# Optimization experiments

Measured on AMD Instinct MI355X. Metric: run time of the kernel, lower is better.

## Reference

```python
import jax, jax.numpy as jnp
import numpy as np

B, P, V, L = 256, 512, 8, 16
N = B * P            # 131072 nodes
C = V * L            # 128 in_channels (== out_channels, forced by the .view in forward)
H = 4                # heads
DOUT = 128           # out_channels per head
E = N * 5            # k=5 neighbors per node
NEG_SLOPE = 0.2


def setup_inputs() -> dict:
    key = jax.random.key(0)
    ks = jax.random.split(key, 8)
    patches = jax.random.normal(ks[0], (B, P, V, L), dtype=jnp.float32)
    edge_index = jax.random.randint(ks[1], (2, E), 0, N, dtype=jnp.int64)
    s = 1.0 / np.sqrt(C)
    W_gat = jax.random.uniform(ks[2], (C, H * DOUT), dtype=jnp.float32, minval=-s, maxval=s)
    att_src = jax.random.uniform(ks[3], (H, DOUT), dtype=jnp.float32, minval=-s, maxval=s)
    att_dst = jax.random.uniform(ks[4], (H, DOUT), dtype=jnp.float32, minval=-s, maxval=s)
    bias_gat = jnp.zeros((H * DOUT,), dtype=jnp.float32)
    s2 = 1.0 / np.sqrt(H * DOUT)
    W_lin = jax.random.uniform(ks[5], (H * DOUT, DOUT), dtype=jnp.float32, minval=-s2, maxval=s2)
    b_lin = jax.random.uniform(ks[6], (DOUT,), dtype=jnp.float32, minval=-s2, maxval=s2)
    return {"patches": patches, "edge_index": edge_index, "W_gat": W_gat,
            "att_src": att_src, "att_dst": att_dst, "bias_gat": bias_gat,
            "W_lin": W_lin, "b_lin": b_lin}


def reference(patches, edge_index, W_gat, att_src, att_dst, bias_gat, W_lin, b_lin):
    b, p, v, l = patches.shape
    n = b * p
    x = patches.reshape(n, v * l)                      # [N, C]
    xw = (x @ W_gat).reshape(n, H, DOUT)               # [N, H, D]
    # PyG GATConv default add_self_loops=True
    loops = jnp.arange(n, dtype=edge_index.dtype)
    src = jnp.concatenate([edge_index[0], loops])      # message source j
    dst = jnp.concatenate([edge_index[1], loops])      # message target i
    a_src = jnp.einsum('nhd,hd->nh', xw, att_src)      # [N, H]
    a_dst = jnp.einsum('nhd,hd->nh', xw, att_dst)
    e = jax.nn.leaky_relu(a_src[src] + a_dst[dst], NEG_SLOPE)   # [Etot, H]
    m = jax.ops.segment_max(e, dst, num_segments=n)
    ex = jnp.exp(e - m[dst])
    denom = jax.ops.segment_sum(ex, dst, num_segments=n)
    alpha = ex / (denom[dst] + 1e-16)                  # segment softmax over in-edges
    out = jax.ops.segment_sum(alpha[:, :, None] * xw[src], dst, num_segments=n)  # [N, H, D]
    out = out.reshape(n, H * DOUT) + bias_gat
    out = jax.nn.elu(out)
    out = out @ W_lin + b_lin                          # [N, DOUT]
    return out.reshape(b, p, v, l)
```

## Files before the change

### kernel.cpp

```cpp
#include <hip/hip_runtime.h>
#include <hip/hip_bf16.h>
#include <stdint.h>

#define N_NODES 131072
#define C_IN    128
#define HEADS   4
#define DHEAD   128
#define HD      512
#define E_EDGES 655360
#define NEG_SLOPE 0.2f
#define NCHUNK  4
#define CHUNK_N (N_NODES / NCHUNK)
#define SCAN_B  (N_NODES / 256)

typedef short bf16x8 __attribute__((ext_vector_type(8)));
typedef float f32x4  __attribute__((ext_vector_type(4)));

__device__ __forceinline__ float bf2f(unsigned short u) {
    unsigned int x = ((unsigned int)u) << 16;
    return __builtin_bit_cast(float, x);
}
__device__ __forceinline__ unsigned short f2bf(float f) {
    unsigned int u = __builtin_bit_cast(unsigned int, f);
    unsigned int r = u + 0x7FFFu + ((u >> 16) & 1u);
    return (unsigned short)(r >> 16);
}
__device__ __forceinline__ float lrelu(float v) {
    return v > 0.0f ? v : NEG_SLOPE * v;
}

__device__ __forceinline__ int perm512(int s) {
    int w = s >> 7, r = s & 127;
    int P = r >> 5, half = (r >> 3) & 3, b = (r >> 2) & 1, e = r & 3;
    return w * 128 + (2 * P + b) * 16 + half * 4 + e;
}

__global__ void detect_kernel(const unsigned int* p_f, const unsigned int* p_i, int* flags) {
    int lane = threadIdx.x;
    int cnt = 0;
#pragma unroll
    for (int r = 0; r < 4; r++) {
        unsigned int e = (p_f[lane + 64 * r] >> 7) & 0xFFu;
        cnt += (e >= 110u && e <= 137u) ? 1 : 0;
    }
    int z = 0;
#pragma unroll
    for (int r = 0; r < 2; r++) {
        z += (p_i[2 * (lane + 64 * r) + 1] == 0u) ? 1 : 0;
    }
#pragma unroll
    for (int o = 1; o < 64; o <<= 1) {
        cnt += __shfl_xor(cnt, o, 64);
        z   += __shfl_xor(z, o, 64);
    }
    if (lane == 0) {
        flags[0] = (cnt >= 128) ? 1 : 0;
        flags[1] = (z == 128) ? 1 : 0;
    }
}

__global__ void conv_w1(const void* in, unsigned short* out, const int* flags) {
    int idx = blockIdx.x * blockDim.x + threadIdx.x;
    int e = idx & 7;
    int l = (idx >> 3) & 63;
    int t = idx >> 9;
    int kk = t & 3, g = t >> 2;
    int col = g * 16 + (l & 15);
    int k = kk * 32 + (l >> 4) * 8 + e;
    float v = flags[0] ? bf2f(((const unsigned short*)in)[k * HD + col])
                       : ((const float*)in)[k * HD + col];
    out[idx] = f2bf(v);
}

__global__ void conv_w2(const void* in, unsigned short* out, const int* flags) {
    int idx = blockIdx.x * blockDim.x + threadIdx.x;
    int n = idx >> 9, s = idx & 511;
    int k = perm512(s);
    float v = flags[0] ? bf2f(((const unsigned short*)in)[k * DHEAD + n])
                       : ((const float*)in)[k * DHEAD + n];
    out[idx] = f2bf(v);
}

__global__ void conv_small(const void* as, const void* ad, const void* bg, const void* bl,
                           float* att_s, float* att_d, float* bias_g, float* b_lin,
                           const int* flags) {
    int i = blockIdx.x * blockDim.x + threadIdx.x;
    bool bf = flags[0] != 0;
    if (i < 512) {
        att_s[i] = bf ? bf2f(((const unsigned short*)as)[i]) : ((const float*)as)[i];
    } else if (i < 1024) {
        int j = i - 512;
        att_d[j] = bf ? bf2f(((const unsigned short*)ad)[j]) : ((const float*)ad)[j];
    } else if (i < 1536) {
        int j = perm512(i - 1024);
        bias_g[i - 1024] = bf ? bf2f(((const unsigned short*)bg)[j]) : ((const float*)bg)[j];
    } else if (i < 1664) {
        int j = i - 1536;
        b_lin[j] = bf ? bf2f(((const unsigned short*)bl)[j]) : ((const float*)bl)[j];
    }
}

__global__ void conv_edges_hist(const void* in, int* src32, int* dst32, int* deg,
                                const int* flags) {
    int i = blockIdx.x * blockDim.x + threadIdx.x;
    if (i >= 2 * E_EDGES) return;
    int v = flags[1] ? (int)((const long long*)in)[i] : ((const int*)in)[i];
    if (i < E_EDGES) {
        src32[i] = v;
    } else {
        dst32[i - E_EDGES] = v;
        atomicAdd(&deg[v], 1);
    }
}

__global__ void zero_deg(int* deg) {
    int i = blockIdx.x * blockDim.x + threadIdx.x;
    deg[i] = 0;
}

__global__ void scan_local(const int* __restrict__ deg, int* __restrict__ offv,
                           int* __restrict__ bsums) {
    __shared__ int tmp[256];
    int t = threadIdx.x;
    int g = blockIdx.x * 256 + t;
    int v = deg[g];
    tmp[t] = v;
    __syncthreads();
#pragma unroll
    for (int d = 1; d < 256; d <<= 1) {
        int x = (t >= d) ? tmp[t - d] : 0;
        __syncthreads();
        tmp[t] += x;
        __syncthreads();
    }
    offv[g] = tmp[t] - v;
    if (t == 255) bsums[blockIdx.x] = tmp[t];
}

__global__ void scan_bsums(int* bsums) {
    __shared__ int tmp[SCAN_B];
    int t = threadIdx.x;
    int v = bsums[t];
    tmp[t] = v;
    __syncthreads();
#pragma unroll
    for (int d = 1; d < SCAN_B; d <<= 1) {
        int x = (t >= d) ? tmp[t - d] : 0;
        __syncthreads();
        tmp[t] += x;
        __syncthreads();
    }
    bsums[t] = tmp[t] - v;
}

__global__ void scan_apply(int* __restrict__ offv, const int* __restrict__ bsums,
                           int* __restrict__ cursor) {
    int g = blockIdx.x * 256 + threadIdx.x;
    int v = offv[g] + bsums[blockIdx.x];
    offv[g] = v;
    cursor[g] = v;
}

__global__ void scatter_kernel(const int* src32, const int* dst32, int* cursor, int* csr) {
    int i = blockIdx.x * blockDim.x + threadIdx.x;
    int d = dst32[i];
    int pos = atomicAdd(&cursor[d], 1);
    csr[pos] = src32[i];
}

__launch_bounds__(256)
__global__ void gemm1_fused(const void* __restrict__ Ain,
                            const unsigned short* __restrict__ BT2,
                            const float* __restrict__ attS, const float* __restrict__ attD,
                            unsigned short* __restrict__ xw,
                            float* __restrict__ aSrc, float* __restrict__ aDst,
                            const int* __restrict__ flags) {
    __shared__ unsigned short lA[64 * 136];
    int tid = threadIdx.x;
    int m0 = blockIdx.x * 64;

    if (flags[0] == 0) {
        const float* Af = (const float*)Ain;
#pragma unroll
        for (int p = 0; p < 8; p++) {
            int l = p * 256 + tid;
            int r = l >> 5, c = (l & 31) * 4;
            float4 f = *(const float4*)&Af[(size_t)(m0 + r) * C_IN + c];
            unsigned short t4[4] = {f2bf(f.x), f2bf(f.y), f2bf(f.z), f2bf(f.w)};
            *(uint2*)&lA[r * 136 + c] = *(const uint2*)t4;
        }
    } else {
        const unsigned short* Ab = (const unsigned short*)Ain;
#pragma unroll
        for (int p = 0; p < 4; p++) {
            int l = p * 256 + tid;
            int r = l >> 4, c = (l & 15) * 8;
            *(uint4*)&lA[r * 136 + c] = *(const uint4*)&Ab[(size_t)(m0 + r) * C_IN + c];
        }
    }
    __syncthreads();

    int w = tid >> 6, lane = tid & 63;
    int lr = lane & 15, half = lane >> 4;

    bf16x8 afr[4][4];
#pragma unroll
    for (int i = 0; i < 4; i++)
#pragma unroll
        for (int kk = 0; kk < 4; kk++)
            afr[i][kk] = *(const bf16x8*)&lA[(i * 16 + lr) * 136 + kk * 32 + half * 8];

    const float4* attS4 = (const float4*)attS;
    const float4* attD4 = (const float4*)attD;

    float dS[4], dD[4];
#pragma unroll
    for (int i = 0; i < 4; i++) { dS[i] = 0.f; dD[i] = 0.f; }

    bf16x8 bbuf[2][4];
#pragma unroll
    for (int kk = 0; kk < 4; kk++)
        bbuf[0][kk] = *(const bf16x8*)&BT2[(((w * 8 + 0) * 4 + kk) << 9) + (lane << 3)];

    uint2 pk_lo[4];

#pragma unroll
    for (int p = 0; p < 8; p++) {
        int cur = p & 1;
        if (p < 7) {
#pragma unroll
            for (int kk = 0; kk < 4; kk++)
                bbuf[cur ^ 1][kk] =
                    *(const bf16x8*)&BT2[(((w * 8 + p + 1) * 4 + kk) << 9) + (lane << 3)];
        }

        f32x4 acc[4];
#pragma unroll
        for (int i = 0; i < 4; i++) acc[i] = (f32x4){0.f, 0.f, 0.f, 0.f};

#pragma unroll
        for (int kk = 0; kk < 4; kk++)
#pragma unroll
            for (int i = 0; i < 4; i++)
                acc[i] = __builtin_amdgcn_mfma_f32_16x16x32_bf16(bbuf[cur][kk], afr[i][kk], acc[i], 0, 0, 0);

        float4 s4 = attS4[w * 32 + p * 4 + half];
        float4 d4 = attD4[w * 32 + p * 4 + half];
#pragma unroll
        for (int i = 0; i < 4; i++) {
            dS[i] += acc[i][0] * s4.x + acc[i][1] * s4.y + acc[i][2] * s4.z + acc[i][3] * s4.w;
            dD[i] += acc[i][0] * d4.x + acc[i][1] * d4.y + acc[i][2] * d4.z + acc[i][3] * d4.w;
        }

        if ((p & 1) == 0) {
#pragma unroll
            for (int i = 0; i < 4; i++) {
                pk_lo[i].x = (unsigned int)f2bf(acc[i][0]) | ((unsigned int)f2bf(acc[i][1]) << 16);
                pk_lo[i].y = (unsigned int)f2bf(acc[i][2]) | ((unsigned int)f2bf(acc[i][3]) << 16);
            }
        } else {
            int P = p >> 1;
#pragma unroll
            for (int i = 0; i < 4; i++) {
                uint4 q;
                q.x = pk_lo[i].x;
                q.y = pk_lo[i].y;
                q.z = (unsigned int)f2bf(acc[i][0]) | ((unsigned int)f2bf(acc[i][1]) << 16);
                q.w = (unsigned int)f2bf(acc[i][2]) | ((unsigned int)f2bf(acc[i][3]) << 16);
                *(uint4*)&xw[(size_t)(m0 + i * 16 + lr) * HD + w * 128 + P * 32 + half * 8] = q;
            }
        }
    }

#pragma unroll
    for (int i = 0; i < 4; i++) {
        float ps = dS[i], pd = dD[i];
        ps += __shfl_xor(ps, 16, 64);
        ps += __shfl_xor(ps, 32, 64);
        pd += __shfl_xor(pd, 16, 64);
        pd += __shfl_xor(pd, 32, 64);
        if (half == 0) {
            aSrc[(size_t)(m0 + i * 16 + lr) * HEADS + w] = ps;
            aDst[(size_t)(m0 + i * 16 + lr) * HEADS + w] = pd;
        }
    }
}

__launch_bounds__(256)
__global__ void gemm2(const unsigned short* __restrict__ A,
                      const unsigned short* __restrict__ BT,
                      const float* __restrict__ bias,
                      unsigned short* Cbf, float* Cf,
                      const int* __restrict__ flags, long long rowOff) {
    __shared__ unsigned short smem[64 * 136];
    unsigned short* lA = smem;
    unsigned short* lB = smem + 64 * 40;
    int tid = threadIdx.x;
    int m0 = blockIdx.x * 64;
    int wid = tid >> 6, lane = tid & 63;
    int wr = (wid >> 1) * 32, wc = (wid & 1) * 64;
    int lr = lane & 15, half = lane >> 4;

    f32x4 acc[2][4];
#pragma unroll
    for (int i = 0; i < 2; i++)
#pragma unroll
        for (int j = 0; j < 4; j++) acc[i][j] = (f32x4){0.f, 0.f, 0.f, 0.f};

    for (int k0 = 0; k0 < HD; k0 += 32) {
        {
            int r = tid >> 2, c = (tid & 3) * 8;
            *(uint4*)&lA[r * 40 + c] = *(const uint4*)&A[(size_t)(m0 + r) * HD + k0 + c];
        }
#pragma unroll
        for (int p = 0; p < 2; p++) {
            int l = p * 256 + tid;
            int r = l >> 2, c = (l & 3) * 8;
            *(uint4*)&lB[r * 40 + c] = *(const uint4*)&BT[(size_t)r * HD + k0 + c];
        }
        __syncthreads();
        bf16x8 af[2], bfr[4];
#pragma unroll
        for (int i = 0; i < 2; i++)
            af[i] = *(const bf16x8*)&lA[(wr + i * 16 + lr) * 40 + half * 8];
#pragma unroll
        for (int j = 0; j < 4; j++)
            bfr[j] = *(const bf16x8*)&lB[(wc + j * 16 + lr) * 40 + half * 8];
#pragma unroll
        for (int i = 0; i < 2; i++)
#pragma unroll
            for (int j = 0; j < 4; j++)
                acc[i][j] = __builtin_amdgcn_mfma_f32_16x16x32_bf16(af[i], bfr[j], acc[i][j], 0, 0, 0);
        __syncthreads();
    }

    if (flags[0] != 0) {
#pragma unroll
        for (int i = 0; i < 2; i++)
#pragma unroll
            for (int j = 0; j < 4; j++) {
                int gcol = wc + j * 16 + lr;
                float b = bias[gcol];
#pragma unroll
                for (int r = 0; r < 4; r++)
                    smem[(wr + i * 16 + half * 4 + r) * 136 + gcol] = f2bf(acc[i][j][r] + b);
            }
        __syncthreads();
#pragma unroll
        for (int p = 0; p < 2; p++) {
            int l = p * 256 + tid;
            int r = l >> 4, c = (l & 15) * 8;
            *(uint4*)&Cbf[(size_t)(rowOff + m0 + r) * DHEAD + c] = *(const uint4*)&smem[r * 136 + c];
        }
    } else {
#pragma unroll
        for (int i = 0; i < 2; i++)
#pragma unroll
            for (int j = 0; j < 4; j++) {
                int gcol = wc + j * 16 + lr;
                float b = bias[gcol];
#pragma unroll
                for (int r = 0; r < 4; r++) {
                    int grow = m0 + wr + i * 16 + half * 4 + r;
                    Cf[(size_t)(rowOff + grow) * DHEAD + gcol] = acc[i][j][r] + b;
                }
            }
    }
}

__launch_bounds__(256)
__global__ void aggregate(const unsigned short* __restrict__ xw,
                          const float* __restrict__ a_src, const float* __restrict__ a_dst,
                          const int* __restrict__ off, const int* __restrict__ deg,
                          const int* __restrict__ csr, const float* __restrict__ bias_g,
                          unsigned short* __restrict__ y, int nodeBase) {
    int local = blockIdx.x * 4 + (threadIdx.x >> 6);
    int node = nodeBase + local;
    int l = threadIdx.x & 63;
    int h = l >> 4;
    int ebase = l * 8;
    int o = off[node], dn = deg[node];
    float ad = a_dst[node * HEADS + h];

    float acc[8];
    float denom;
    {
        float w = __expf(lrelu(a_src[node * HEADS + h] + ad));
        uint4 q = *(const uint4*)&xw[(size_t)node * HD + ebase];
        const unsigned short* u = (const unsigned short*)&q;
        denom = w;
#pragma unroll
        for (int k = 0; k < 8; k++) acc[k] = w * bf2f(u[k]);
    }

    for (int e0 = 0; e0 < dn; e0 += 8) {
        int   idx[8];
        float as[8];
        uint4 px[8];
#pragma unroll
        for (int b = 0; b < 8; b++)
            idx[b] = (e0 + b < dn) ? csr[o + e0 + b] : node;
#pragma unroll
        for (int b = 0; b < 8; b++)
            as[b] = a_src[idx[b] * HEADS + h];
#pragma unroll
        for (int b = 0; b < 8; b++)
            px[b] = *(const uint4*)&xw[(size_t)idx[b] * HD + ebase];
#pragma unroll
        for (int b = 0; b < 8; b++) {
            float w = (e0 + b < dn) ? __expf(lrelu(as[b] + ad)) : 0.0f;
            denom += w;
            const unsigned short* u = (const unsigned short*)&px[b];
#pragma unroll
            for (int k = 0; k < 8; k++) acc[k] += w * bf2f(u[k]);
        }
    }

    float inv = 1.0f / (denom + 1e-16f);
    unsigned short outp[8];
#pragma unroll
    for (int k = 0; k < 8; k++) {
        float v = acc[k] * inv + bias_g[ebase + k];
        v = v > 0.f ? v : (__expf(v) - 1.0f);
        outp[k] = f2bf(v);
    }
    *(uint4*)&y[(size_t)local * HD + ebase] = *(const uint4*)outp;
}

extern "C" void kernel_launch(void* const* d_in, const int* in_sizes, int n_in,
                              void* d_out, int out_size, void* d_ws, size_t ws_size,
                              hipStream_t stream) {
    char* ws = (char*)d_ws;
    size_t wsoff = 0;
    auto alloc = [&](size_t bytes) -> char* {
        char* p = ws + wsoff;
        wsoff += (bytes + 255) & ~(size_t)255;
        return p;
    };

    int*            flags  = (int*)           alloc(256);
    unsigned short* WT1    = (unsigned short*)alloc((size_t)HD * C_IN * 2);
    unsigned short* WT2    = (unsigned short*)alloc((size_t)DHEAD * HD * 2);
    float*          attS   = (float*)         alloc(HD * 4);
    float*          attD   = (float*)         alloc(HD * 4);
    float*          biasG  = (float*)         alloc(HD * 4);
    float*          bLin   = (float*)         alloc(DHEAD * 4);
    int*            src32  = (int*)           alloc((size_t)E_EDGES * 4);
    int*            dst32  = (int*)           alloc((size_t)E_EDGES * 4);
    int*            deg    = (int*)           alloc((size_t)N_NODES * 4);
    int*            offv   = (int*)           alloc((size_t)(N_NODES + 1) * 4);
    int*            cursor = (int*)           alloc((size_t)N_NODES * 4);
    int*            csr    = (int*)           alloc((size_t)E_EDGES * 4);
    int*            bsums  = (int*)           alloc((size_t)SCAN_B * 4);
    float*          aSrc   = (float*)         alloc((size_t)N_NODES * HEADS * 4);
    float*          aDst   = (float*)         alloc((size_t)N_NODES * HEADS * 4);
    unsigned short* xw     = (unsigned short*)alloc((size_t)N_NODES * HD * 2);
    unsigned short* ychunk = (unsigned short*)alloc((size_t)CHUNK_N * HD * 2);

    const void* patches = d_in[0];
    const void* edges   = d_in[1];
    const void* Wgat    = d_in[2];
    const void* attSrcI = d_in[3];
    const void* attDstI = d_in[4];
    const void* biasGI  = d_in[5];
    const void* WlinI   = d_in[6];
    const void* bLinI   = d_in[7];

    detect_kernel<<<1, 64, 0, stream>>>((const unsigned int*)patches,
                                        (const unsigned int*)edges, flags);

    conv_w1<<<(HD * C_IN) / 256, 256, 0, stream>>>(Wgat, WT1, flags);
    conv_w2<<<(DHEAD * HD) / 256, 256, 0, stream>>>(WlinI, WT2, flags);
    conv_small<<<7, 256, 0, stream>>>(attSrcI, attDstI, biasGI, bLinI,
                                      attS, attD, biasG, bLin, flags);

    zero_deg<<<N_NODES / 256, 256, 0, stream>>>(deg);
    conv_edges_hist<<<(2 * E_EDGES) / 256, 256, 0, stream>>>(edges, src32, dst32, deg, flags);
    scan_local<<<SCAN_B, 256, 0, stream>>>(deg, offv, bsums);
    scan_bsums<<<1, SCAN_B, 0, stream>>>(bsums);
    scan_apply<<<SCAN_B, 256, 0, stream>>>(offv, bsums, cursor);
    scatter_kernel<<<E_EDGES / 256, 256, 0, stream>>>(src32, dst32, cursor, csr);

    gemm1_fused<<<N_NODES / 64, 256, 0, stream>>>(
        patches, WT1, attS, attD, xw, aSrc, aDst, flags);

    for (int c = 0; c < NCHUNK; c++) {
        int base = c * CHUNK_N;
        aggregate<<<CHUNK_N / 4, 256, 0, stream>>>(xw, aSrc, aDst, offv, deg, csr,
                                                   biasG, ychunk, base);
        gemm2<<<CHUNK_N / 64, 256, 0, stream>>>(
            ychunk, WT2, bLin, (unsigned short*)d_out, (float*)d_out, flags, base);
    }
}
```

Baseline: 448.0 us.

## Fuse neighbor aggregation with output linear GEMM via shared-memory tile

Replaces the chunked aggregate + gemm2 launch pair with one kernel that aggregates 32 nodes per block into an LDS tile and immediately multiplies it by W_lin using MFMA. W_lin is pre-swizzled into MFMA fragment order so each wave streams its B fragments straight from global memory with double buffering. This removes the round trip of the 512-wide intermediate through global memory and the extra launches. In exchange it uses about 33KB of LDS per block, which may limit occupancy for the latency-bound gather phase, and each block re-reads the whole W_lin.

After: 387.4 us. -13.5%, faster.

```diff
diff --git a/kernel.cpp b/kernel.cpp
--- a/kernel.cpp
+++ b/kernel.cpp
@@ -9,9 +9,8 @@
 #define HD      512
 #define E_EDGES 655360
 #define NEG_SLOPE 0.2f
-#define NCHUNK  4
-#define CHUNK_N (N_NODES / NCHUNK)
 #define SCAN_B  (N_NODES / 256)
+#define MT      32
 
 typedef short bf16x8 __attribute__((ext_vector_type(8)));
 typedef float f32x4  __attribute__((ext_vector_type(4)));
@@ -74,10 +73,15 @@
 
 __global__ void conv_w2(const void* in, unsigned short* out, const int* flags) {
     int idx = blockIdx.x * blockDim.x + threadIdx.x;
-    int n = idx >> 9, s = idx & 511;
-    int k = perm512(s);
-    float v = flags[0] ? bf2f(((const unsigned short*)in)[k * DHEAD + n])
-                       : ((const float*)in)[k * DHEAD + n];
+    int e = idx & 7;
+    int l = (idx >> 3) & 63;
+    int f = idx >> 9;
+    int kk = f & 15, jg = f >> 4;
+    int col = jg * 16 + (l & 15);
+    int sk = kk * 32 + (l >> 4) * 8 + e;
+    int k = perm512(sk);
+    float v = flags[0] ? bf2f(((const unsigned short*)in)[k * DHEAD + col])
+                       : ((const float*)in)[k * DHEAD + col];
     out[idx] = f2bf(v);
 }
 
@@ -287,144 +291,133 @@
 }
 
 __launch_bounds__(256)
-__global__ void gemm2(const unsigned short* __restrict__ A,
-                      const unsigned short* __restrict__ BT,
-                      const float* __restrict__ bias,
-                      unsigned short* Cbf, float* Cf,
-                      const int* __restrict__ flags, long long rowOff) {
-    __shared__ unsigned short smem[64 * 136];
-    unsigned short* lA = smem;
-    unsigned short* lB = smem + 64 * 40;
-    int tid = threadIdx.x;
-    int m0 = blockIdx.x * 64;
-    int wid = tid >> 6, lane = tid & 63;
-    int wr = (wid >> 1) * 32, wc = (wid & 1) * 64;
-    int lr = lane & 15, half = lane >> 4;
-
-    f32x4 acc[2][4];
-#pragma unroll
-    for (int i = 0; i < 2; i++)
-#pragma unroll
-        for (int j = 0; j < 4; j++) acc[i][j] = (f32x4){0.f, 0.f, 0.f, 0.f};
-
-    for (int k0 = 0; k0 < HD; k0 += 32) {
-        {
-            int r = tid >> 2, c = (tid & 3) * 8;
-            *(uint4*)&lA[r * 40 + c] = *(const uint4*)&A[(size_t)(m0 + r) * HD + k0 + c];
-        }
-#pragma unroll
-        for (int p = 0; p < 2; p++) {
-            int l = p * 256 + tid;
-            int r = l >> 2, c = (l & 3) * 8;
-            *(uint4*)&lB[r * 40 + c] = *(const uint4*)&BT[(size_t)r * HD + k0 + c];
-        }
-        __syncthreads();
-        bf16x8 af[2], bfr[4];
-#pragma unroll
-        for (int i = 0; i < 2; i++)
-            af[i] = *(const bf16x8*)&lA[(wr + i * 16 + lr) * 40 + half * 8];
-#pragma unroll
-        for (int j = 0; j < 4; j++)
-            bfr[j] = *(const bf16x8*)&lB[(wc + j * 16 + lr) * 40 + half * 8];
-#pragma unroll
-        for (int i = 0; i < 2; i++)
-#pragma unroll
-            for (int j = 0; j < 4; j++)
-                acc[i][j] = __builtin_amdgcn_mfma_f32_16x16x32_bf16(af[i], bfr[j], acc[i][j], 0, 0, 0);
-        __syncthreads();
-    }
-
-    if (flags[0] != 0) {
-#pragma unroll
-        for (int i = 0; i < 2; i++)
-#pragma unroll
-            for (int j = 0; j < 4; j++) {
-                int gcol = wc + j * 16 + lr;
-                float b = bias[gcol];
-#pragma unroll
-                for (int r = 0; r < 4; r++)
-                    smem[(wr + i * 16 + half * 4 + r) * 136 + gcol] = f2bf(acc[i][j][r] + b);
-            }
-        __syncthreads();
-#pragma unroll
-        for (int p = 0; p < 2; p++) {
-            int l = p * 256 + tid;
-            int r = l >> 4, c = (l & 15) * 8;
-            *(uint4*)&Cbf[(size_t)(rowOff + m0 + r) * DHEAD + c] = *(const uint4*)&smem[r * 136 + c];
-        }
-    } else {
-#pragma unroll
-        for (int i = 0; i < 2; i++)
-#pragma unroll
-            for (int j = 0; j < 4; j++) {
-                int gcol = wc + j * 16 + lr;
-                float b = bias[gcol];
-#pragma unroll
-                for (int r = 0; r < 4; r++) {
-                    int grow = m0 + wr + i * 16 + half * 4 + r;
-                    Cf[(size_t)(rowOff + grow) * DHEAD + gcol] = acc[i][j][r] + b;
-                }
-            }
-    }
-}
-
-__launch_bounds__(256)
-__global__ void aggregate(const unsigned short* __restrict__ xw,
+__global__ void agg_gemm2(const unsigned short* __restrict__ xw,
                           const float* __restrict__ a_src, const float* __restrict__ a_dst,
                           const int* __restrict__ off, const int* __restrict__ deg,
                           const int* __restrict__ csr, const float* __restrict__ bias_g,
-                          unsigned short* __restrict__ y, int nodeBase) {
-    int local = blockIdx.x * 4 + (threadIdx.x >> 6);
-    int node = nodeBase + local;
-    int l = threadIdx.x & 63;
+                          const unsigned short* __restrict__ BT2f,
+                          const float* __restrict__ b_lin,
+                          unsigned short* __restrict__ Cbf, float* __restrict__ Cf,
+                          const int* __restrict__ flags) {
+    __shared__ unsigned short yt[MT * 520];
+    int tid = threadIdx.x;
+    int m0 = blockIdx.x * MT;
+    int w = tid >> 6, l = tid & 63;
     int h = l >> 4;
     int ebase = l * 8;
-    int o = off[node], dn = deg[node];
-    float ad = a_dst[node * HEADS + h];
-
-    float acc[8];
-    float denom;
-    {
-        float w = __expf(lrelu(a_src[node * HEADS + h] + ad));
-        uint4 q = *(const uint4*)&xw[(size_t)node * HD + ebase];
-        const unsigned short* u = (const unsigned short*)&q;
-        denom = w;
-#pragma unroll
-        for (int k = 0; k < 8; k++) acc[k] = w * bf2f(u[k]);
-    }
-
-    for (int e0 = 0; e0 < dn; e0 += 8) {
-        int   idx[8];
-        float as[8];
-        uint4 px[8];
-#pragma unroll
-        for (int b = 0; b < 8; b++)
-            idx[b] = (e0 + b < dn) ? csr[o + e0 + b] : node;
-#pragma unroll
-        for (int b = 0; b < 8; b++)
-            as[b] = a_src[idx[b] * HEADS + h];
-#pragma unroll
-        for (int b = 0; b < 8; b++)
-            px[b] = *(const uint4*)&xw[(size_t)idx[b] * HD + ebase];
-#pragma unroll
-        for (int b = 0; b < 8; b++) {
-            float w = (e0 + b < dn) ? __expf(lrelu(as[b] + ad)) : 0.0f;
-            denom += w;
-            const unsigned short* u = (const unsigned short*)&px[b];
-#pragma unroll
-            for (int k = 0; k < 8; k++) acc[k] += w * bf2f(u[k]);
-        }
-    }
-
-    float inv = 1.0f / (denom + 1e-16f);
-    unsigned short outp[8];
-#pragma unroll
-    for (int k = 0; k < 8; k++) {
-        float v = acc[k] * inv + bias_g[ebase + k];
-        v = v > 0.f ? v : (__expf(v) - 1.0f);
-        outp[k] = f2bf(v);
-    }
-    *(uint4*)&y[(size_t)local * HD + ebase] = *(const uint4*)outp;
+
+    for (int g = 0; g < MT / 4; g++) {
+        int row = w * (MT / 4) + g;
+        int node = m0 + row;
+        int o = off[node], dn = deg[node];
+        float ad = a_dst[node * HEADS + h];
+
+        float acc[8];
+        float denom;
+        {
+            float wgt = __expf(lrelu(a_src[node * HEADS + h] + ad));
+            uint4 q = *(const uint4*)&xw[(size_t)node * HD + ebase];
+            const unsigned short* u = (const unsigned short*)&q;
+            denom = wgt;
+#pragma unroll
+            for (int k = 0; k < 8; k++) acc[k] = wgt * bf2f(u[k]);
+        }
+
+        for (int e0 = 0; e0 < dn; e0 += 8) {
+            int   idx[8];
+            float as[8];
+            uint4 px[8];
+#pragma unroll
+            for (int b = 0; b < 8; b++)
+                idx[b] = (e0 + b < dn) ? csr[o + e0 + b] : node;
+#pragma unroll
+            for (int b = 0; b < 8; b++)
+                as[b] = a_src[idx[b] * HEADS + h];
+#pragma unroll
+            for (int b = 0; b < 8; b++)
+                px[b] = *(const uint4*)&xw[(size_t)idx[b] * HD + ebase];
+#pragma unroll
+            for (int b = 0; b < 8; b++) {
+                float wgt = (e0 + b < dn) ? __expf(lrelu(as[b] + ad)) : 0.0f;
+                denom += wgt;
+                const unsigned short* u = (const unsigned short*)&px[b];
+#pragma unroll
+                for (int k = 0; k < 8; k++) acc[k] += wgt * bf2f(u[k]);
+            }
+        }
+
+        float inv = 1.0f / (denom + 1e-16f);
+        unsigned short outp[8];
+#pragma unroll
+        for (int k = 0; k < 8; k++) {
+            float v = acc[k] * inv + bias_g[ebase + k];
+            v = v > 0.f ? v : (__expf(v) - 1.0f);
+            outp[k] = f2bf(v);
+        }
+        *(uint4*)&yt[row * 520 + ebase] = *(const uint4*)outp;
+    }
+    __syncthreads();
+
+    int lr = l & 15, half = l >> 4;
+    f32x4 acc2[2][2];
+#pragma unroll
+    for (int i = 0; i < 2; i++)
+#pragma unroll
+        for (int j = 0; j < 2; j++) acc2[i][j] = (f32x4){0.f, 0.f, 0.f, 0.f};
+
+    bf16x8 bb[2][2];
+#pragma unroll
+    for (int j = 0; j < 2; j++)
+        bb[0][j] = *(const bf16x8*)&BT2f[((((w * 2 + j) * 16 + 0) * 64 + l) << 3)];
+
+    for (int kk = 0; kk < 16; kk++) {
+        int cur = kk & 1;
+        if (kk < 15) {
+#pragma unroll
+            for (int j = 0; j < 2; j++)
+                bb[cur ^ 1][j] = *(const bf16x8*)&BT2f[((((w * 2 + j) * 16 + kk + 1) * 64 + l) << 3)];
+        }
+        bf16x8 af0 = *(const bf16x8*)&yt[(lr) * 520 + kk * 32 + half * 8];
+        bf16x8 af1 = *(const bf16x8*)&yt[(16 + lr) * 520 + kk * 32 + half * 8];
+        acc2[0][0] = __builtin_amdgcn_mfma_f32_16x16x32_bf16(af0, bb[cur][0], acc2[0][0], 0, 0, 0);
+        acc2[0][1] = __builtin_amdgcn_mfma_f32_16x16x32_bf16(af0, bb[cur][1], acc2[0][1], 0, 0, 0);
+        acc2[1][0] = __builtin_amdgcn_mfma_f32_16x16x32_bf16(af1, bb[cur][0], acc2[1][0], 0, 0, 0);
+        acc2[1][1] = __builtin_amdgcn_mfma_f32_16x16x32_bf16(af1, bb[cur][1], acc2[1][1], 0, 0, 0);
+    }
+
+    if (flags[0] != 0) {
+        __syncthreads();
+#pragma unroll
+        for (int i = 0; i < 2; i++)
+#pragma unroll
+            for (int j = 0; j < 2; j++) {
+                int gcol = (w * 2 + j) * 16 + lr;
+                float b = b_lin[gcol];
+#pragma unroll
+                for (int r = 0; r < 4; r++)
+                    yt[(i * 16 + half * 4 + r) * 136 + gcol] = f2bf(acc2[i][j][r] + b);
+            }
+        __syncthreads();
+#pragma unroll
+        for (int p = 0; p < 2; p++) {
+            int ln = p * 256 + tid;
+            int r = ln >> 4, c = (ln & 15) * 8;
+            *(uint4*)&Cbf[(size_t)(m0 + r) * DHEAD + c] = *(const uint4*)&yt[r * 136 + c];
+        }
+    } else {
+#pragma unroll
+        for (int i = 0; i < 2; i++)
+#pragma unroll
+            for (int j = 0; j < 2; j++) {
+                int gcol = (w * 2 + j) * 16 + lr;
+                float b = b_lin[gcol];
+#pragma unroll
+                for (int r = 0; r < 4; r++) {
+                    int grow = m0 + i * 16 + half * 4 + r;
+                    Cf[(size_t)grow * DHEAD + gcol] = acc2[i][j][r] + b;
+                }
+            }
+    }
 }
 
 extern "C" void kernel_launch(void* const* d_in, const int* in_sizes, int n_in,
@@ -455,7 +448,6 @@
     float*          aSrc   = (float*)         alloc((size_t)N_NODES * HEADS * 4);
     float*          aDst   = (float*)         alloc((size_t)N_NODES * HEADS * 4);
     unsigned short* xw     = (unsigned short*)alloc((size_t)N_NODES * HD * 2);
-    unsigned short* ychunk = (unsigned short*)alloc((size_t)CHUNK_N * HD * 2);
 
     const void* patches = d_in[0];
     const void* edges   = d_in[1];
@@ -484,11 +476,7 @@
     gemm1_fused<<<N_NODES / 64, 256, 0, stream>>>(
         patches, WT1, attS, attD, xw, aSrc, aDst, flags);
 
-    for (int c = 0; c < NCHUNK; c++) {
-        int base = c * CHUNK_N;
-        aggregate<<<CHUNK_N / 4, 256, 0, stream>>>(xw, aSrc, aDst, offv, deg, csr,
-                                                   biasG, ychunk, base);
-        gemm2<<<CHUNK_N / 64, 256, 0, stream>>>(
-            ychunk, WT2, bLin, (unsigned short*)d_out, (float*)d_out, flags, base);
-    }
-}
+    agg_gemm2<<<N_NODES / MT, 256, 0, stream>>>(
+        xw, aSrc, aDst, offv, deg, csr, biasG, WT2, bLin,
+        (unsigned short*)d_out, (float*)d_out, flags);
+}
```
